# Performance work log

Measured on AMD Instinct MI355X. Metric: run time of the kernel, lower is better.

## Reference

```python
import jax, jax.numpy as jnp
import numpy as np
from collections import deque


def _build_graph_paths(N, E, seed=0):
    """Random directed graph; all-pairs BFS shortest paths (matches nx.shortest_path on
    the unweighted DiGraph). Returns flattened (pair_id, node_id) membership lists:
    for every reachable pair (i,j) and every node e on the shortest path i->j, one
    entry with pair_id=i*N+j, node_id=e. path_len[i*N+j] = number of nodes on the
    path (0 if unreachable)."""
    rng = np.random.default_rng(seed)
    src = rng.integers(0, N, E)
    dst = rng.integers(0, N, E)
    adj = [[] for _ in range(N)]
    for u, v in zip(src, dst):
        adj[u].append(int(v))
    pair_chunks, node_chunks = [], []
    path_len = np.zeros(N * N, dtype=np.int32)
    for s in range(N):
        dist = np.full(N, -1, np.int32)
        parent = np.full(N, -1, np.int32)
        dist[s] = 0
        parent[s] = s
        q = deque([s])
        while q:
            u = q.popleft()
            for v in adj[u]:
                if dist[v] < 0:
                    dist[v] = dist[u] + 1
                    parent[v] = u
                    q.append(v)
        reach = np.nonzero(dist >= 0)[0].astype(np.int32)
        path_len[s * N + reach] = dist[reach] + 1
        cur = reach.copy()
        rem = dist[reach].copy()          # steps remaining (records rem+1 nodes)
        pid = (s * N + reach).astype(np.int64)
        while cur.size:
            pair_chunks.append(pid.copy())
            node_chunks.append(cur.copy())
            m = rem > 0                   # keep walking toward the source
            cur = parent[cur[m]]
            rem = rem[m] - 1
            pid = pid[m]
    pair_id = np.concatenate(pair_chunks).astype(np.int32)
    node_id = np.concatenate(node_chunks).astype(np.int32)
    return pair_id, node_id, path_len


def setup_inputs() -> dict:
    N, DIM, H, E = 1024, 64, 16, 8192
    pair_id, node_id, path_len = _build_graph_paths(N, E, seed=0)
    key = jax.random.key(0)
    k1, k2, k3, k4 = jax.random.split(key, 4)
    x = jax.random.normal(k1, (N, DIM), jnp.float32)
    edge_attr = jax.random.normal(k2, (N, 4), jnp.float32)
    lim = 1.0 / np.sqrt(4.0)              # nn.Linear(4, H) default init range
    W = jax.random.uniform(k3, (H, 4), jnp.float32, -lim, lim)
    b = jax.random.uniform(k4, (H,), jnp.float32, -lim, lim)
    return {
        "x": x,
        "edge_attr": edge_attr,
        "W": W,
        "b": b,
        "pair_id": jnp.asarray(pair_id),
        "node_id": jnp.asarray(node_id),
        "path_len": jnp.asarray(path_len),
    }


def reference(x, edge_attr, W, b, pair_id, node_id, path_len):
    # Original: out[i,j] = mean_{e in shortest_path(i,j)} (W @ edge_attr[e] + b),
    # 0 where no path. Implemented as gather + segment_sum + one small GEMM
    # (exactly equal by linearity of the Linear layer).
    N = x.shape[0]
    H = W.shape[0]
    gathered = edge_attr[node_id]                                   # [P, 4]
    sums = jax.ops.segment_sum(gathered, pair_id, num_segments=N * N)  # [N*N, 4]
    L = path_len[:, None].astype(sums.dtype)                        # [N*N, 1]
    lin = sums @ W.T + L * b                                        # sum of per-node Linear outputs
    out = jnp.where(path_len[:, None] > 0, lin / jnp.maximum(L, 1.0), 0.0)
    out = out.reshape(N, N, H)
    return jnp.transpose(out, (2, 0, 1))                            # 'h w n -> n h w'
```

## Files before the change

### kernel.cpp

```cpp
#include <hip/hip_runtime.h>


#define BS 512
#define NMAX 1024
#define NW (BS / 64)

__global__ __launch_bounds__(BS) void ee_fused(
    const float* __restrict__ edge_attr,
    const float* __restrict__ W,
    const float* __restrict__ b,
    const int*   __restrict__ pair_id,
    const int*   __restrict__ node_id,
    const int*   __restrict__ path_len,
    float*       __restrict__ out,
    int N, int NN, int P)
{
    __shared__ __align__(16) float4 sea[NMAX];
    __shared__ __align__(16) float4 psum[NMAX];
    __shared__ float sW[64];
    __shared__ float sbv[16];
    __shared__ int wsA0[NW], wsA1[NW], wsB0[NW], wsB1[NW];
    __shared__ int slo, smaxd;

    const int tid   = threadIdx.x;
    const int wave  = tid >> 6;
    const int lane  = tid & 63;
    const int s     = blockIdx.x;
    const int sbase = s * N;

    if (tid == 0) { smaxd = 0; slo = 0; }
    for (int i = tid; i < N; i += BS)
        sea[i] = reinterpret_cast<const float4*>(edge_attr)[i];
    if (tid < 64) sW[tid]  = W[tid];
    if (tid < 16) sbv[tid] = b[tid];

    const int j0 = tid, j1 = tid + BS;
    const int L0 = (j0 < N) ? path_len[sbase + j0] : 0;
    const int L1 = (j1 < N) ? path_len[sbase + j1] : 0;

    if (wave == 0 && P > 0) {
        int lo = 0, hi = P;
        while (hi > lo) {
            const int span = hi - lo;
            const int p = lo + (int)(((long long)span * lane) >> 6);
            const int v = pair_id[p];
            const unsigned long long bal = __ballot(v >= sbase);
            if (bal == 0ull) {
                lo += (int)(((long long)span * 63) >> 6) + 1;
            } else {
                const int f = (int)__builtin_ctzll(bal);
                if (f == 0) {
                    hi = lo;
                } else {
                    const int pf   = lo + (int)(((long long)span * f) >> 6);
                    const int pfm1 = lo + (int)(((long long)span * (f - 1)) >> 6);
                    lo = pfm1 + 1;
                    hi = pf;
                }
            }
        }
        if (lane == 0) slo = lo;
    }
    __syncthreads();
    const int lo = slo;

    const unsigned long long bA0 = __ballot(L0 > 1);
    const unsigned long long bA1 = __ballot(L1 > 1);
    const unsigned long long bB0 = __ballot(L0 > 0);
    const unsigned long long bB1 = __ballot(L1 > 0);
    int m = max(L0, L1);
    for (int o = 32; o > 0; o >>= 1) m = max(m, __shfl_down(m, o));
    if (lane == 0) {
        wsA0[wave] = __popcll(bA0);
        wsA1[wave] = __popcll(bA1);
        wsB0[wave] = __popcll(bB0);
        wsB1[wave] = __popcll(bB1);
        atomicMax(&smaxd, m);
    }
    __syncthreads();
    int preA0 = 0, totA0 = 0, preA1 = 0, n0 = 0;
#pragma unroll
    for (int w = 0; w < NW; ++w) {
        const int a0 = wsA0[w], a1 = wsA1[w];
        totA0 += a0;
        if (w < wave) { preA0 += a0; preA1 += a1; }
        n0 += wsB0[w] + wsB1[w];
    }
    const unsigned long long below = (1ull << lane) - 1ull;
    const int rank0 = preA0 + __popcll(bA0 & below);
    const int rank1 = totA0 + preA1 + __popcll(bA1 & below);
    const int maxd = smaxd;

    int par0 = 0, par1 = 0;
    if (L0 > 1) par0 = node_id[lo + n0 + rank0];
    if (L1 > 1) par1 = node_id[lo + n0 + rank1];

    float4 acc0 = make_float4(0.f, 0.f, 0.f, 0.f), acc1 = acc0;
    for (int d = 0; d < maxd; ++d) {
        if (L0 == d + 1) {
            float4 e = sea[j0];
            if (d) { const float4 q = psum[par0]; e.x += q.x; e.y += q.y; e.z += q.z; e.w += q.w; }
            acc0 = e; psum[j0] = e;
        }
        if (L1 == d + 1) {
            float4 e = sea[j1];
            if (d) { const float4 q = psum[par1]; e.x += q.x; e.y += q.y; e.z += q.z; e.w += q.w; }
            acc1 = e; psum[j1] = e;
        }
        __syncthreads();
    }

    const float f0 = (L0 > 0) ? 1.0f / (float)L0 : 0.0f;
    const float f1 = (L1 > 0) ? 1.0f / (float)L1 : 0.0f;
    const float g0 = (L0 > 0) ? 1.0f : 0.0f;
    const float g1 = (L1 > 0) ? 1.0f : 0.0f;
#pragma unroll
    for (int h = 0; h < 16; ++h) {
        const float w0 = sW[4 * h + 0], w1 = sW[4 * h + 1];
        const float w2 = sW[4 * h + 2], w3 = sW[4 * h + 3];
        const float bh = sbv[h];
        float* o = out + (size_t)h * NN + sbase;
        if (j0 < N)
            __builtin_nontemporal_store(
                (acc0.x * w0 + acc0.y * w1 + acc0.z * w2 + acc0.w * w3) * f0 + bh * g0,
                o + j0);
        if (j1 < N)
            __builtin_nontemporal_store(
                (acc1.x * w0 + acc1.y * w1 + acc1.z * w2 + acc1.w * w3) * f1 + bh * g1,
                o + j1);
    }
}

extern "C" void kernel_launch(void* const* d_in, const int* in_sizes, int n_in,
                              void* d_out, int out_size, void* d_ws, size_t ws_size,
                              hipStream_t stream) {
    const float* edge_attr = (const float*)d_in[1];
    const float* W         = (const float*)d_in[2];
    const float* b         = (const float*)d_in[3];
    const int*   pair_id   = (const int*)d_in[4];
    const int*   node_id   = (const int*)d_in[5];
    const int*   path_len  = (const int*)d_in[6];
    const int P  = in_sizes[4];
    const int NN = in_sizes[6];
    const int N  = in_sizes[0] / 64;

    ee_fused<<<N, BS, 0, stream>>>(edge_attr, W, b, pair_id, node_id, path_len,
                                   (float*)d_out, N, NN, P);
}
```

Baseline: 114.9 us.

## Shrink blocks to 256 threads and emit outputs inside the depth loop

Block size drops to 256 threads, each handling four targets, with a launch bound of 8 blocks per CU. The shared edge_attr staging is removed and rows are read straight from global memory. Each output row is stored as soon as its depth level finishes, instead of in a final pass after the loop. Prefix counts now come from per-(k,wave) shared counters, replacing the atomicMax and one barrier. The aim is higher occupancy, less shared memory and stores spread across the levels, but each level now does uneven store work before its barrier.

```diff
diff --git a/kernel.cpp b/kernel.cpp
--- a/kernel.cpp
+++ b/kernel.cpp
@@ -1,11 +1,15 @@
 #include <hip/hip_runtime.h>
 
 
-#define BS 512
+#define BS 256
+#define NW 4
+#define KPT 4
 #define NMAX 1024
-#define NW (BS / 64)
+#define NG (KPT * NW)
 
-__global__ __launch_bounds__(BS) void ee_fused(
+typedef float f32x4 __attribute__((ext_vector_type(4)));
+
+__global__ __launch_bounds__(BS, 8) void ee_fused(
     const float* __restrict__ edge_attr,
     const float* __restrict__ W,
     const float* __restrict__ b,
@@ -15,12 +19,13 @@
     float*       __restrict__ out,
     int N, int NN, int P)
 {
-    __shared__ __align__(16) float4 sea[NMAX];
-    __shared__ __align__(16) float4 psum[NMAX];
+    __shared__ __align__(16) f32x4 psum[NMAX];
     __shared__ float sW[64];
     __shared__ float sbv[16];
-    __shared__ int wsA0[NW], wsA1[NW], wsB0[NW], wsB1[NW];
-    __shared__ int slo, smaxd;
+    __shared__ int scnt1[NG];
+    __shared__ int scnt0[NG];
+    __shared__ int smaxw[NW];
+    __shared__ int slo;
 
     const int tid   = threadIdx.x;
     const int wave  = tid >> 6;
@@ -28,15 +33,30 @@
     const int s     = blockIdx.x;
     const int sbase = s * N;
 
-    if (tid == 0) { smaxd = 0; slo = 0; }
-    for (int i = tid; i < N; i += BS)
-        sea[i] = reinterpret_cast<const float4*>(edge_attr)[i];
+    if (tid == 0) slo = 0;
     if (tid < 64) sW[tid]  = W[tid];
     if (tid < 16) sbv[tid] = b[tid];
 
-    const int j0 = tid, j1 = tid + BS;
-    const int L0 = (j0 < N) ? path_len[sbase + j0] : 0;
-    const int L1 = (j1 < N) ? path_len[sbase + j1] : 0;
+    int L[KPT];
+#pragma unroll
+    for (int k = 0; k < KPT; ++k) {
+        const int j = k * BS + tid;
+        L[k] = (j < N) ? path_len[sbase + j] : 0;
+    }
+
+    int m = 0;
+#pragma unroll
+    for (int k = 0; k < KPT; ++k) {
+        m = max(m, L[k]);
+        const unsigned long long b1 = __ballot(L[k] > 1);
+        const unsigned long long b0 = __ballot(L[k] > 0);
+        if (lane == 0) {
+            scnt1[k * NW + wave] = __popcll(b1);
+            scnt0[k * NW + wave] = __popcll(b0);
+        }
+    }
+    for (int o = 32; o > 0; o >>= 1) m = max(m, __shfl_down(m, o));
+    if (lane == 0) smaxw[wave] = m;
 
     if (wave == 0 && P > 0) {
         int lo = 0, hi = P;
@@ -64,70 +84,53 @@
     __syncthreads();
     const int lo = slo;
 
-    const unsigned long long bA0 = __ballot(L0 > 1);
-    const unsigned long long bA1 = __ballot(L1 > 1);
-    const unsigned long long bB0 = __ballot(L0 > 0);
-    const unsigned long long bB1 = __ballot(L1 > 0);
-    int m = max(L0, L1);
-    for (int o = 32; o > 0; o >>= 1) m = max(m, __shfl_down(m, o));
-    if (lane == 0) {
-        wsA0[wave] = __popcll(bA0);
-        wsA1[wave] = __popcll(bA1);
-        wsB0[wave] = __popcll(bB0);
-        wsB1[wave] = __popcll(bB1);
-        atomicMax(&smaxd, m);
+    int n0 = 0, maxd = 0;
+#pragma unroll
+    for (int g = 0; g < NG; ++g) n0 += scnt0[g];
+#pragma unroll
+    for (int w = 0; w < NW; ++w) maxd = max(maxd, smaxw[w]);
+
+    const unsigned long long below = (1ull << lane) - 1ull;
+    int par[KPT];
+#pragma unroll
+    for (int k = 0; k < KPT; ++k) {
+        par[k] = 0;
+        const unsigned long long b1 = __ballot(L[k] > 1);
+        if (L[k] > 1) {
+            int pre = 0;
+            const int gme = k * NW + wave;
+#pragma unroll
+            for (int g = 0; g < NG; ++g)
+                if (g < gme) pre += scnt1[g];
+            const int rank = pre + __popcll(b1 & below);
+            par[k] = node_id[lo + n0 + rank];
+        }
     }
-    __syncthreads();
-    int preA0 = 0, totA0 = 0, preA1 = 0, n0 = 0;
+
+    for (int d = 0; d < maxd; ++d) {
 #pragma unroll
-    for (int w = 0; w < NW; ++w) {
-        const int a0 = wsA0[w], a1 = wsA1[w];
-        totA0 += a0;
-        if (w < wave) { preA0 += a0; preA1 += a1; }
-        n0 += wsB0[w] + wsB1[w];
-    }
-    const unsigned long long below = (1ull << lane) - 1ull;
-    const int rank0 = preA0 + __popcll(bA0 & below);
-    const int rank1 = totA0 + preA1 + __popcll(bA1 & below);
-    const int maxd = smaxd;
-
-    int par0 = 0, par1 = 0;
-    if (L0 > 1) par0 = node_id[lo + n0 + rank0];
-    if (L1 > 1) par1 = node_id[lo + n0 + rank1];
-
-    float4 acc0 = make_float4(0.f, 0.f, 0.f, 0.f), acc1 = acc0;
-    for (int d = 0; d < maxd; ++d) {
-        if (L0 == d + 1) {
-            float4 e = sea[j0];
-            if (d) { const float4 q = psum[par0]; e.x += q.x; e.y += q.y; e.z += q.z; e.w += q.w; }
-            acc0 = e; psum[j0] = e;
-        }
-        if (L1 == d + 1) {
-            float4 e = sea[j1];
-            if (d) { const float4 q = psum[par1]; e.x += q.x; e.y += q.y; e.z += q.z; e.w += q.w; }
-            acc1 = e; psum[j1] = e;
+        for (int k = 0; k < KPT; ++k) {
+            const int j = k * BS + tid;
+            if (L[k] == d + 1) {
+                f32x4 e = *reinterpret_cast<const f32x4*>(edge_attr + 4 * j);
+                if (d) e += psum[par[k]];
+                psum[j] = e;
+                const float f = 1.0f / (float)L[k];
+                float* o = out + sbase + j;
+#pragma unroll
+                for (int h = 0; h < 16; ++h)
+                    __builtin_nontemporal_store(
+                        (e.x * sW[4 * h + 0] + e.y * sW[4 * h + 1] +
+                         e.z * sW[4 * h + 2] + e.w * sW[4 * h + 3]) * f + sbv[h],
+                        o + (size_t)h * NN);
+            } else if (d == 0 && L[k] == 0 && j < N) {
+                float* o = out + sbase + j;
+#pragma unroll
+                for (int h = 0; h < 16; ++h)
+                    __builtin_nontemporal_store(0.0f, o + (size_t)h * NN);
+            }
         }
         __syncthreads();
-    }
-
-    const float f0 = (L0 > 0) ? 1.0f / (float)L0 : 0.0f;
-    const float f1 = (L1 > 0) ? 1.0f / (float)L1 : 0.0f;
-    const float g0 = (L0 > 0) ? 1.0f : 0.0f;
-    const float g1 = (L1 > 0) ? 1.0f : 0.0f;
-#pragma unroll
-    for (int h = 0; h < 16; ++h) {
-        const float w0 = sW[4 * h + 0], w1 = sW[4 * h + 1];
-        const float w2 = sW[4 * h + 2], w3 = sW[4 * h + 3];
-        const float bh = sbv[h];
-        float* o = out + (size_t)h * NN + sbase;
-        if (j0 < N)
-            __builtin_nontemporal_store(
-                (acc0.x * w0 + acc0.y * w1 + acc0.z * w2 + acc0.w * w3) * f0 + bh * g0,
-                o + j0);
-        if (j1 < N)
-            __builtin_nontemporal_store(
-                (acc1.x * w0 + acc1.y * w1 + acc1.z * w2 + acc1.w * w3) * f1 + bh * g1,
-                o + j1);
     }
 }
 
```

After: 247.5 us. 2.15x slower.
